# Optimization experiments

Hardware: AMD Instinct MI355X
Metric: run time of the kernel (lower is better)

The kernel has to match this reference:

```python
import jax, jax.numpy as jnp
import numpy as np

NEG_INF = -100000000.0  # matches masked_fill value in torch source

def setup_inputs() -> dict:
    key = jax.random.key(0)
    ks = jax.random.split(key, 7)
    d_model, d = 1024, 128
    B, S = 4, 2048
    scale = 1.0 / np.sqrt(d_model)
    x = jax.random.normal(ks[0], (B, S, d_model), dtype=jnp.float32)
    Wq = jax.random.normal(ks[1], (d, d_model), dtype=jnp.float32) * scale
    bq = jax.random.normal(ks[2], (d,), dtype=jnp.float32) * 0.02
    Wk = jax.random.normal(ks[3], (d, d_model), dtype=jnp.float32) * scale
    bk = jax.random.normal(ks[4], (d,), dtype=jnp.float32) * 0.02
    Wv = jax.random.normal(ks[5], (d, d_model), dtype=jnp.float32) * scale
    bv = jax.random.normal(ks[6], (d,), dtype=jnp.float32) * 0.02
    return {"x": x, "Wq": Wq, "bq": bq, "Wk": Wk, "bk": bk, "Wv": Wv, "bv": bv}

def reference(x, Wq, bq, Wk, bk, Wv, bv):
    # Q,K,V: [B,S,d] via torch Linear (x @ W.T + b)
    Q = jnp.einsum('bsm,dm->bsd', x, Wq) + bq
    K = jnp.einsum('bsm,dm->bsd', x, Wk) + bk
    V = jnp.einsum('bsm,dm->bsd', x, Wv) + bv
    d = Wk.shape[0]
    scale = 1.0 / jnp.sqrt(jnp.asarray(d, dtype=Q.dtype))
    scores = jnp.einsum('bqd,bkd->bqk', Q, K) * scale  # [B,S,S]
    # Faithful to source: tril then value-based mask (tril==0 -> -1e8).
    tril = jnp.tril(scores)
    masked = jnp.where(tril == 0, NEG_INF, tril)
    attn = jax.nn.softmax(masked, axis=-1)
    context = jnp.einsum('bqk,bkd->bqd', attn, V)
    return context
```

## Files before the change

kernel.cpp:

```cpp
#include <hip/hip_runtime.h>

typedef __attribute__((ext_vector_type(8))) short bf16x8;
typedef __attribute__((ext_vector_type(4))) float f32x4;

__device__ __forceinline__ unsigned short f2bf(float f) {
    unsigned int u = __float_as_uint(f);
    u += 0x7fffu + ((u >> 16) & 1u);
    return (unsigned short)(u >> 16);
}
__device__ __forceinline__ float bf2f(unsigned short h) {
    return __uint_as_float((unsigned int)h << 16);
}
__device__ __forceinline__ unsigned int pack2bf(float lo, float hi) {
    return (unsigned int)f2bf(lo) | ((unsigned int)f2bf(hi) << 16);
}
__device__ __forceinline__ unsigned int cvtpk(float a, float b) {
    unsigned int r;
    asm("v_cvt_pk_bf16_f32 %0, %1, %2" : "=v"(r) : "v"(a), "v"(b));
    return r;
}
__device__ __forceinline__ void async_ld16(void* lds, const void* g) {
    __builtin_amdgcn_global_load_lds(
        (const __attribute__((address_space(1))) unsigned int*)g,
        (__attribute__((address_space(3))) unsigned int*)lds, 16, 0, 0);
}

__global__ __launch_bounds__(256) void conv_w(
    const float* __restrict__ Wq, const float* __restrict__ Wk,
    const float* __restrict__ Wv, unsigned short* __restrict__ Wcat)
{
    size_t o = ((size_t)blockIdx.x * 256 + threadIdx.x) * 8;
    int sel = (int)(o >> 17);
    const float* W = (sel == 0) ? Wq : ((sel == 1) ? Wk : Wv);
    const float* src = W + (o & 131071);
    float4 f0 = ((const float4*)src)[0];
    float4 f1 = ((const float4*)src)[1];
    uint4 u;
    u.x = pack2bf(f0.x, f0.y); u.y = pack2bf(f0.z, f0.w);
    u.z = pack2bf(f1.x, f1.y); u.w = pack2bf(f1.z, f1.w);
    *(uint4*)(Wcat + o) = u;
}

__global__ __launch_bounds__(256, 3) void qkv_gemm(
    const float* __restrict__ x,
    const unsigned short* __restrict__ Wcat,
    const float* __restrict__ bq, const float* __restrict__ bk,
    const float* __restrict__ bv,
    unsigned short* __restrict__ Qf,
    unsigned short* __restrict__ Kf,
    unsigned short* __restrict__ Vf)
{
    __shared__ float Asf[2][32 * 64];
    __shared__ unsigned short Bs[2][128 * 64];

    const int tid  = threadIdx.x;
    const int lane = tid & 63;
    const int w    = tid >> 6;
    const int quad = lane >> 4;
    const int ln   = lane & 15;
    const int lr   = lane >> 3;
    const int csw  = ((lane & 7) ^ lr) * 8;

    const int bid   = blockIdx.x;
    const int nb    = bid >> 8;
    const int mbase = (bid & 255) * 32;
    const unsigned short* Wsel = Wcat + (size_t)nb * 128 * 1024;

    const int g0 = tid, g1 = tid + 256;
    const float* asrc0 = x + (size_t)(mbase + (g0 >> 4)) * 1024
                           + (size_t)(((g0 & 15) ^ ((g0 >> 4) & 15)) * 4);
    const float* asrc1 = x + (size_t)(mbase + (g1 >> 4)) * 1024
                           + (size_t)(((g1 & 15) ^ ((g1 >> 4) & 15)) * 4);

    f32x4 acc[2][2];
#pragma unroll
    for (int mt = 0; mt < 2; mt++)
#pragma unroll
        for (int nt = 0; nt < 2; nt++) acc[mt][nt] = (f32x4){0.f, 0.f, 0.f, 0.f};

    auto stageB = [&](int kb, int p) {
        const int kcol = kb * 64 + csw;
#pragma unroll
        for (int j = 0; j < 4; j++) {
            int chunk = w * 4 + j;
            async_ld16(&Bs[p][chunk * 512 + lane * 8],
                       Wsel + (size_t)(chunk * 8 + lr) * 1024 + kcol);
        }
    };
    auto stageA = [&](int kb, int p) {
        async_ld16(&Asf[p][g0 * 4], asrc0 + kb * 64);
        async_ld16(&Asf[p][g1 * 4], asrc1 + kb * 64);
    };
    auto readA = [&](int p, int mt, int ks) -> bf16x8 {
        const int r = mt * 16 + ln;
        const int J = ks * 4 + quad;
        float4 lo = *(const float4*)&Asf[p][r * 64 + (((2 * J)    ) ^ (r & 15)) * 4];
        float4 hi = *(const float4*)&Asf[p][r * 64 + (((2 * J + 1)) ^ (r & 15)) * 4];
        uint4 u = { cvtpk(lo.x, lo.y), cvtpk(lo.z, lo.w),
                    cvtpk(hi.x, hi.y), cvtpk(hi.z, hi.w) };
        return *reinterpret_cast<const bf16x8*>(&u);
    };

    stageB(0, 0);
    stageA(0, 0);
    __syncthreads();

    for (int kb = 0; kb < 16; kb++) {
        const int p = kb & 1;
        if (kb < 15) {
            stageB(kb + 1, p ^ 1);
            stageA(kb + 1, p ^ 1);
        }
#pragma unroll
        for (int ks = 0; ks < 2; ks++) {
            bf16x8 a[2], b[2];
#pragma unroll
            for (int mt = 0; mt < 2; mt++) a[mt] = readA(p, mt, ks);
#pragma unroll
            for (int nt = 0; nt < 2; nt++) {
                int row = w * 32 + nt * 16 + ln;
                b[nt] = *(const bf16x8*)&Bs[p][row * 64 + ((ks * 4 + quad) ^ (ln & 7)) * 8];
            }
#pragma unroll
            for (int mt = 0; mt < 2; mt++)
#pragma unroll
                for (int nt = 0; nt < 2; nt++)
                    acc[mt][nt] = __builtin_amdgcn_mfma_f32_16x16x32_bf16(
                        a[mt], b[nt], acc[mt][nt], 0, 0, 0);
        }
        __syncthreads();
    }

    const float scale = (nb == 0) ? 0.08838834764831845f : 1.0f;
    const float* bsel = (nb == 0) ? bq : ((nb == 1) ? bk : bv);
    float bias_v[2];
#pragma unroll
    for (int nt = 0; nt < 2; nt++) bias_v[nt] = bsel[w * 32 + nt * 16 + ln];

    if (nb == 0) {
#pragma unroll
        for (int mt = 0; mt < 2; mt++)
#pragma unroll
            for (int nt = 0; nt < 2; nt++)
#pragma unroll
                for (int r = 0; r < 4; r++) {
                    int m = mbase + mt * 16 + quad * 4 + r;
                    int d = w * 32 + nt * 16 + ln;
                    int bb = m >> 11, s = m & 2047;
                    int qq = s >> 6, j = s & 63, wv = j >> 4, lnq = j & 15;
                    int ksd = d >> 5, rr = d & 31, qd = rr >> 3, e = rr & 7;
                    size_t idx = (((size_t)((bb * 32 + qq) * 4 + wv) * 4 + ksd) * 64
                                  + qd * 16 + lnq) * 8 + e;
                    Qf[idx] = f2bf((acc[mt][nt][r] + bias_v[nt]) * scale);
                }
    } else if (nb == 1) {
#pragma unroll
        for (int mt = 0; mt < 2; mt++)
#pragma unroll
            for (int nt = 0; nt < 2; nt++)
#pragma unroll
                for (int r = 0; r < 4; r++) {
                    int m = mbase + mt * 16 + quad * 4 + r;
                    int d = w * 32 + nt * 16 + ln;
                    int bb = m >> 11, s = m & 2047;
                    int kt = s >> 6, j = s & 63, ct = j >> 4, lnk = j & 15;
                    int ksd = d >> 5, rr = d & 31, qd = rr >> 3, e = rr & 7;
                    size_t idx = (((size_t)(bb * 128 + kt * 4 + ct) * 4 + ksd) * 64
                                  + qd * 16 + lnk) * 8 + e;
                    Kf[idx] = f2bf(acc[mt][nt][r] + bias_v[nt]);
                }
    } else {
#pragma unroll
        for (int mt = 0; mt < 2; mt++)
#pragma unroll
            for (int nt = 0; nt < 2; nt++) {
                int dd = w * 32 + nt * 16 + ln;
                int m0 = mbase + mt * 16 + quad * 4;
                int bb = m0 >> 11, s0 = m0 & 2047;
                int kt = s0 >> 6, j0 = s0 & 63;
                int kstep = j0 >> 5, rr0 = j0 & 31, qdv = rr0 >> 3, e0 = rr0 & 7;
                int dt = dd >> 4, lnv = dd & 15;
                size_t base = ((((size_t)(bb * 32 + kt) * 2 + kstep) * 8 + dt) * 64
                               + qdv * 16 + lnv) * 8 + e0;
                ushort4 u = { f2bf(acc[mt][nt][0] + bias_v[nt]),
                              f2bf(acc[mt][nt][1] + bias_v[nt]),
                              f2bf(acc[mt][nt][2] + bias_v[nt]),
                              f2bf(acc[mt][nt][3] + bias_v[nt]) };
                *(ushort4*)&Vf[base] = u;
            }
    }
}

__global__ __launch_bounds__(64, 2) void flash_attn(
    const unsigned short* __restrict__ Qf,
    const unsigned short* __restrict__ Kf,
    const unsigned short* __restrict__ Vf,
    unsigned short* __restrict__ Opart,
    float* __restrict__ lsum_g,
    float* __restrict__ out)
{
    __shared__ unsigned short Pl[16][72];

    const int w = blockIdx.x & 3;
    int j = blockIdx.x >> 2;
    const int b = j / 144;
    int t = j % 144;
    int q = 0, c = 0;
#pragma unroll 1
    for (int qq = 0; qq < 32; qq++) {
        int ncq = (qq >> 2) + 1;
        if (t < ncq) { q = qq; c = t; break; }
        t -= ncq;
    }
    const int m4 = q >> 2, r4 = q & 3;
    const int nc = m4 + 1;
    const int pbase = b * 144 + q + 2 * m4 * (m4 - 1) + r4 * m4;
    const int pidx  = pbase + c;
    const int k0 = c * 4;
    const int kend = (c * 4 + 4 < q + 1) ? (c * 4 + 4) : (q + 1);

    const int lane = threadIdx.x & 63, quad = lane >> 4, ln = lane & 15;
    const float M0 = 16.0f;

    bf16x8 qa[4];
    const unsigned short* qbt =
        Qf + (size_t)((b * 32 + q) * 4 + w) * 2048 + lane * 8;
#pragma unroll
    for (int ks = 0; ks < 4; ks++)
        qa[ks] = *(const bf16x8*)(qbt + (size_t)ks * 512);

    float l_i[4];
    f32x4 Ofr[8];
#pragma unroll
    for (int r = 0; r < 4; r++) l_i[r] = 0.f;
#pragma unroll
    for (int dt = 0; dt < 8; dt++) Ofr[dt] = (f32x4){0.f, 0.f, 0.f, 0.f};

    for (int kt = k0; kt < kend; kt++) {
        const unsigned short* kbt = Kf + (size_t)(b * 128 + kt * 4) * 2048 + lane * 8;
        const unsigned short* vbt = Vf + (size_t)(b * 32 + kt) * 8192 + lane * 8;
        bf16x8 kf[4][4], vf[2][8];
#pragma unroll
        for (int ct = 0; ct < 4; ct++)
#pragma unroll
            for (int ks = 0; ks < 4; ks++)
                kf[ct][ks] = *(const bf16x8*)(kbt + (size_t)(ct * 4 + ks) * 512);
#pragma unroll
        for (int kstep = 0; kstep < 2; kstep++)
#pragma unroll
            for (int dt = 0; dt < 8; dt++)
                vf[kstep][dt] = *(const bf16x8*)(vbt + (size_t)(kstep * 8 + dt) * 512);

        f32x4 sfr[4];
#pragma unroll
        for (int ct = 0; ct < 4; ct++) {
            f32x4 s = (f32x4){0.f, 0.f, 0.f, 0.f};
#pragma unroll
            for (int ks = 0; ks < 4; ks++)
                s = __builtin_amdgcn_mfma_f32_16x16x32_bf16(qa[ks], kf[ct][ks], s, 0, 0, 0);
            sfr[ct] = s;
        }

        if (kt == q) {
#pragma unroll
            for (int ct = 0; ct < 4; ct++)
#pragma unroll
                for (int r = 0; r < 4; r++)
                    if (ct * 16 + ln > w * 16 + quad * 4 + r)
                        sfr[ct][r] = -__builtin_inff();
        }

#pragma unroll
        for (int ct = 0; ct < 4; ct++)
#pragma unroll
            for (int r = 0; r < 4; r++) {
                float pv = __expf(sfr[ct][r] - M0);
                l_i[r] += pv;
                Pl[quad * 4 + r][ct * 16 + ln] = f2bf(pv);
            }

#pragma unroll
        for (int kstep = 0; kstep < 2; kstep++) {
            bf16x8 pa = *(const bf16x8*)&Pl[ln][kstep * 32 + quad * 8];
#pragma unroll
            for (int dt = 0; dt < 8; dt++)
                Ofr[dt] = __builtin_amdgcn_mfma_f32_16x16x32_bf16(pa, vf[kstep][dt], Ofr[dt], 0, 0, 0);
        }
    }

#pragma unroll
    for (int off = 1; off < 16; off <<= 1)
#pragma unroll
        for (int r = 0; r < 4; r++) l_i[r] += __shfl_xor(l_i[r], off, 64);

    if (nc == 1) {
        float inv_[4];
#pragma unroll
        for (int r = 0; r < 4; r++) inv_[r] = 1.0f / l_i[r];
#pragma unroll
        for (int dt = 0; dt < 8; dt++)
#pragma unroll
            for (int r = 0; r < 4; r++) {
                int row = w * 16 + quad * 4 + r;
                out[((size_t)(b * 2048 + q * 64 + row)) * 128 + dt * 16 + ln] =
                    Ofr[dt][r] * inv_[r];
            }
        return;
    }

#pragma unroll
    for (int dt = 0; dt < 8; dt++) {
        ushort4 u = { f2bf(Ofr[dt][0]), f2bf(Ofr[dt][1]),
                      f2bf(Ofr[dt][2]), f2bf(Ofr[dt][3]) };
        *(ushort4*)&Opart[(((size_t)pidx * 8 + dt) * 4 + w) * 256 + lane * 4] = u;
    }
    if (ln == 0) {
#pragma unroll
        for (int r = 0; r < 4; r++)
            lsum_g[(size_t)pidx * 64 + w * 16 + quad * 4 + r] = l_i[r];
    }
}

__global__ __launch_bounds__(256) void combine(
    const unsigned short* __restrict__ Opart,
    const float* __restrict__ lsum_g,
    float* __restrict__ out)
{
    const int j = blockIdx.x;
    const int b = j / 28;
    const int q = (j % 28) + 4;
    const int m4 = q >> 2, r4 = q & 3;
    const int nc = m4 + 1;
    const int pbase = b * 144 + q + 2 * m4 * (m4 - 1) + r4 * m4;

    const int tid  = threadIdx.x;
    const int lane = tid & 63, w = tid >> 6, quad = lane >> 4, ln = lane & 15;

    float lt[4] = {0.f, 0.f, 0.f, 0.f};
    f32x4 Ofr[8];
#pragma unroll
    for (int dt = 0; dt < 8; dt++) Ofr[dt] = (f32x4){0.f, 0.f, 0.f, 0.f};

#pragma unroll 1
    for (int c2 = 0; c2 < nc; c2++) {
        const size_t pb2 = (size_t)(pbase + c2);
#pragma unroll
        for (int r = 0; r < 4; r++)
            lt[r] += lsum_g[pb2 * 64 + w * 16 + quad * 4 + r];
#pragma unroll
        for (int dt = 0; dt < 8; dt++) {
            ushort4 u = *(const ushort4*)&Opart[((pb2 * 8 + dt) * 4 + w) * 256 + lane * 4];
            Ofr[dt][0] += bf2f(u.x);
            Ofr[dt][1] += bf2f(u.y);
            Ofr[dt][2] += bf2f(u.z);
            Ofr[dt][3] += bf2f(u.w);
        }
    }
    float inv_[4];
#pragma unroll
    for (int r = 0; r < 4; r++) inv_[r] = 1.0f / lt[r];
#pragma unroll
    for (int dt = 0; dt < 8; dt++)
#pragma unroll
        for (int r = 0; r < 4; r++) {
            int row = w * 16 + quad * 4 + r;
            out[((size_t)(b * 2048 + q * 64 + row)) * 128 + dt * 16 + ln] =
                Ofr[dt][r] * inv_[r];
        }
}

extern "C" void kernel_launch(void* const* d_in, const int* in_sizes, int n_in,
                              void* d_out, int out_size, void* d_ws, size_t ws_size,
                              hipStream_t stream) {
    const float* x  = (const float*)d_in[0];
    const float* Wq = (const float*)d_in[1];
    const float* bq = (const float*)d_in[2];
    const float* Wk = (const float*)d_in[3];
    const float* bk = (const float*)d_in[4];
    const float* Wv = (const float*)d_in[5];
    const float* bv = (const float*)d_in[6];
    float* out = (float*)d_out;

    char* wsb = (char*)d_ws;
    unsigned short* Opart = (unsigned short*)wsb;
    float*          lsum  = (float*)(wsb + 9437184);
    unsigned short* Wcat  = (unsigned short*)(wsb + 10485760);
    unsigned short* Qf    = (unsigned short*)(wsb + 11272192);
    unsigned short* Kf    = Qf + (size_t)8192 * 128;
    unsigned short* Vf    = Qf + (size_t)2 * 8192 * 128;

    conv_w<<<192, 256, 0, stream>>>(Wq, Wk, Wv, Wcat);
    qkv_gemm<<<768, 256, 0, stream>>>(x, Wcat, bq, bk, bv, Qf, Kf, Vf);
    flash_attn<<<2304, 64, 0, stream>>>(Qf, Kf, Vf, Opart, lsum, out);
    combine<<<112, 256, 0, stream>>>(Opart, lsum, out);
}
```

Baseline: 118.8 us.

## Stage x via registers with bf16 conversion before LDS in QKV GEMM

The QKV projection now loads fp32 x tiles into registers, converts them to bf16 once, and writes them to a swizzled bf16 LDS buffer. Previously the fp32 tiles were async-copied to LDS and each wave converted them on every read. This halves A-tile LDS footprint and removes redundant conversions across the four waves, but the global load is now synchronous through registers instead of async direct-to-LDS. The launch-bounds occupancy hint is also dropped, and the weight conversion kernel now uses the packed bf16 convert instruction.

```diff
diff --git a/kernel.cpp b/kernel.cpp
--- a/kernel.cpp
+++ b/kernel.cpp
@@ -10,9 +10,6 @@
 }
 __device__ __forceinline__ float bf2f(unsigned short h) {
     return __uint_as_float((unsigned int)h << 16);
-}
-__device__ __forceinline__ unsigned int pack2bf(float lo, float hi) {
-    return (unsigned int)f2bf(lo) | ((unsigned int)f2bf(hi) << 16);
 }
 __device__ __forceinline__ unsigned int cvtpk(float a, float b) {
     unsigned int r;
@@ -36,12 +33,12 @@
     float4 f0 = ((const float4*)src)[0];
     float4 f1 = ((const float4*)src)[1];
     uint4 u;
-    u.x = pack2bf(f0.x, f0.y); u.y = pack2bf(f0.z, f0.w);
-    u.z = pack2bf(f1.x, f1.y); u.w = pack2bf(f1.z, f1.w);
+    u.x = cvtpk(f0.x, f0.y); u.y = cvtpk(f0.z, f0.w);
+    u.z = cvtpk(f1.x, f1.y); u.w = cvtpk(f1.z, f1.w);
     *(uint4*)(Wcat + o) = u;
 }
 
-__global__ __launch_bounds__(256, 3) void qkv_gemm(
+__global__ __launch_bounds__(256) void qkv_gemm(
     const float* __restrict__ x,
     const unsigned short* __restrict__ Wcat,
     const float* __restrict__ bq, const float* __restrict__ bk,
@@ -50,7 +47,7 @@
     unsigned short* __restrict__ Kf,
     unsigned short* __restrict__ Vf)
 {
-    __shared__ float Asf[2][32 * 64];
+    __shared__ unsigned short As[2][32 * 64];
     __shared__ unsigned short Bs[2][128 * 64];
 
     const int tid  = threadIdx.x;
@@ -66,11 +63,12 @@
     const int mbase = (bid & 255) * 32;
     const unsigned short* Wsel = Wcat + (size_t)nb * 128 * 1024;
 
-    const int g0 = tid, g1 = tid + 256;
-    const float* asrc0 = x + (size_t)(mbase + (g0 >> 4)) * 1024
-                           + (size_t)(((g0 & 15) ^ ((g0 >> 4) & 15)) * 4);
-    const float* asrc1 = x + (size_t)(mbase + (g1 >> 4)) * 1024
-                           + (size_t)(((g1 & 15) ^ ((g1 >> 4) & 15)) * 4);
+    const int arow  = tid >> 3;
+    const int achk  = tid & 7;
+    const int aslot = achk ^ (arow & 7);
+    const float* xsrc = x + (size_t)(mbase + arow) * 1024 + achk * 8;
+    unsigned short* adst0 = &As[0][arow * 64 + aslot * 8];
+    unsigned short* adst1 = &As[1][arow * 64 + aslot * 8];
 
     f32x4 acc[2][2];
 #pragma unroll
@@ -87,35 +85,36 @@
                        Wsel + (size_t)(chunk * 8 + lr) * 1024 + kcol);
         }
     };
-    auto stageA = [&](int kb, int p) {
-        async_ld16(&Asf[p][g0 * 4], asrc0 + kb * 64);
-        async_ld16(&Asf[p][g1 * 4], asrc1 + kb * 64);
+    auto writeA = [&](int p, const float4& f0, const float4& f1) {
+        uint4 u;
+        u.x = cvtpk(f0.x, f0.y); u.y = cvtpk(f0.z, f0.w);
+        u.z = cvtpk(f1.x, f1.y); u.w = cvtpk(f1.z, f1.w);
+        *(uint4*)((p == 0) ? adst0 : adst1) = u;
     };
-    auto readA = [&](int p, int mt, int ks) -> bf16x8 {
-        const int r = mt * 16 + ln;
-        const int J = ks * 4 + quad;
-        float4 lo = *(const float4*)&Asf[p][r * 64 + (((2 * J)    ) ^ (r & 15)) * 4];
-        float4 hi = *(const float4*)&Asf[p][r * 64 + (((2 * J + 1)) ^ (r & 15)) * 4];
-        uint4 u = { cvtpk(lo.x, lo.y), cvtpk(lo.z, lo.w),
-                    cvtpk(hi.x, hi.y), cvtpk(hi.z, hi.w) };
-        return *reinterpret_cast<const bf16x8*>(&u);
-    };
-
+
+    float4 a0 = ((const float4*)xsrc)[0];
+    float4 a1 = ((const float4*)xsrc)[1];
     stageB(0, 0);
-    stageA(0, 0);
+    writeA(0, a0, a1);
     __syncthreads();
 
     for (int kb = 0; kb < 16; kb++) {
         const int p = kb & 1;
+        float4 n0, n1;
         if (kb < 15) {
             stageB(kb + 1, p ^ 1);
-            stageA(kb + 1, p ^ 1);
+            const float* xs = xsrc + (kb + 1) * 64;
+            n0 = ((const float4*)xs)[0];
+            n1 = ((const float4*)xs)[1];
         }
 #pragma unroll
         for (int ks = 0; ks < 2; ks++) {
             bf16x8 a[2], b[2];
 #pragma unroll
-            for (int mt = 0; mt < 2; mt++) a[mt] = readA(p, mt, ks);
+            for (int mt = 0; mt < 2; mt++) {
+                int row = mt * 16 + ln;
+                a[mt] = *(const bf16x8*)&As[p][row * 64 + ((ks * 4 + quad) ^ (ln & 7)) * 8];
+            }
 #pragma unroll
             for (int nt = 0; nt < 2; nt++) {
                 int row = w * 32 + nt * 16 + ln;
@@ -128,6 +127,7 @@
                     acc[mt][nt] = __builtin_amdgcn_mfma_f32_16x16x32_bf16(
                         a[mt], b[nt], acc[mt][nt], 0, 0, 0);
         }
+        if (kb < 15) writeA(p ^ 1, n0, n1);
         __syncthreads();
     }
 
```

Result: no change. 121.0 us (+1.8%).

## Split QKV GEMM tile across 8 waves and use hardware bf16 pack in weight conversion

Applied to the files above, without the earlier changes.

The QKV projection GEMM block grows from 4 to 8 waves arranged 2x4 over the same 32x128 output tile, so each wave computes one 16-row strip with two MFMA accumulators instead of four. Each thread now issues half as many async global-to-LDS loads per stage. The aim is more latency hiding and better spread of staging work, at the cost of more waves per block and lower MFMA work per wave. The weight conversion kernel also switches from software rounding to the v_cvt_pk_bf16_f32 instruction.

```diff
diff --git a/kernel.cpp b/kernel.cpp
--- a/kernel.cpp
+++ b/kernel.cpp
@@ -10,9 +10,6 @@
 }
 __device__ __forceinline__ float bf2f(unsigned short h) {
     return __uint_as_float((unsigned int)h << 16);
-}
-__device__ __forceinline__ unsigned int pack2bf(float lo, float hi) {
-    return (unsigned int)f2bf(lo) | ((unsigned int)f2bf(hi) << 16);
 }
 __device__ __forceinline__ unsigned int cvtpk(float a, float b) {
     unsigned int r;
@@ -36,12 +33,12 @@
     float4 f0 = ((const float4*)src)[0];
     float4 f1 = ((const float4*)src)[1];
     uint4 u;
-    u.x = pack2bf(f0.x, f0.y); u.y = pack2bf(f0.z, f0.w);
-    u.z = pack2bf(f1.x, f1.y); u.w = pack2bf(f1.z, f1.w);
+    u.x = cvtpk(f0.x, f0.y); u.y = cvtpk(f0.z, f0.w);
+    u.z = cvtpk(f1.x, f1.y); u.w = cvtpk(f1.z, f1.w);
     *(uint4*)(Wcat + o) = u;
 }
 
-__global__ __launch_bounds__(256, 3) void qkv_gemm(
+__global__ __launch_bounds__(512, 4) void qkv_gemm(
     const float* __restrict__ x,
     const unsigned short* __restrict__ Wcat,
     const float* __restrict__ bq, const float* __restrict__ bk,
@@ -56,6 +53,8 @@
     const int tid  = threadIdx.x;
     const int lane = tid & 63;
     const int w    = tid >> 6;
+    const int wm   = w >> 2;
+    const int wn   = w & 3;
     const int quad = lane >> 4;
     const int ln   = lane & 15;
     const int lr   = lane >> 3;
@@ -64,35 +63,30 @@
     const int bid   = blockIdx.x;
     const int nb    = bid >> 8;
     const int mbase = (bid & 255) * 32;
-    const unsigned short* Wsel = Wcat + (size_t)nb * 128 * 1024;
-
-    const int g0 = tid, g1 = tid + 256;
-    const float* asrc0 = x + (size_t)(mbase + (g0 >> 4)) * 1024
-                           + (size_t)(((g0 & 15) ^ ((g0 >> 4) & 15)) * 4);
-    const float* asrc1 = x + (size_t)(mbase + (g1 >> 4)) * 1024
-                           + (size_t)(((g1 & 15) ^ ((g1 >> 4) & 15)) * 4);
-
-    f32x4 acc[2][2];
-#pragma unroll
-    for (int mt = 0; mt < 2; mt++)
-#pragma unroll
-        for (int nt = 0; nt < 2; nt++) acc[mt][nt] = (f32x4){0.f, 0.f, 0.f, 0.f};
+    const unsigned short* Wsel = Wcat + (size_t)nb * 131072;
+
+    const int g = tid;
+    const float* asrc = x + (size_t)(mbase + (g >> 4)) * 1024
+                          + (size_t)(((g & 15) ^ ((g >> 4) & 15)) * 4);
+
+    f32x4 acc[2];
+#pragma unroll
+    for (int nt = 0; nt < 2; nt++) acc[nt] = (f32x4){0.f, 0.f, 0.f, 0.f};
 
     auto stageB = [&](int kb, int p) {
         const int kcol = kb * 64 + csw;
 #pragma unroll
-        for (int j = 0; j < 4; j++) {
-            int chunk = w * 4 + j;
+        for (int j = 0; j < 2; j++) {
+            int chunk = w * 2 + j;
             async_ld16(&Bs[p][chunk * 512 + lane * 8],
                        Wsel + (size_t)(chunk * 8 + lr) * 1024 + kcol);
         }
     };
     auto stageA = [&](int kb, int p) {
-        async_ld16(&Asf[p][g0 * 4], asrc0 + kb * 64);
-        async_ld16(&Asf[p][g1 * 4], asrc1 + kb * 64);
+        async_ld16(&Asf[p][g * 4], asrc + kb * 64);
     };
-    auto readA = [&](int p, int mt, int ks) -> bf16x8 {
-        const int r = mt * 16 + ln;
+    auto readA = [&](int p, int ks) -> bf16x8 {
+        const int r = wm * 16 + ln;
         const int J = ks * 4 + quad;
         float4 lo = *(const float4*)&Asf[p][r * 64 + (((2 * J)    ) ^ (r & 15)) * 4];
         float4 hi = *(const float4*)&Asf[p][r * 64 + (((2 * J + 1)) ^ (r & 15)) * 4];
@@ -113,20 +107,15 @@
         }
 #pragma unroll
         for (int ks = 0; ks < 2; ks++) {
-            bf16x8 a[2], b[2];
-#pragma unroll
-            for (int mt = 0; mt < 2; mt++) a[mt] = readA(p, mt, ks);
-#pragma unroll
-            for (int nt = 0; nt < 2; nt++) {
-                int row = w * 32 + nt * 16 + ln;
-                b[nt] = *(const bf16x8*)&Bs[p][row * 64 + ((ks * 4 + quad) ^ (ln & 7)) * 8];
-            }
-#pragma unroll
-            for (int mt = 0; mt < 2; mt++)
-#pragma unroll
-                for (int nt = 0; nt < 2; nt++)
-                    acc[mt][nt] = __builtin_amdgcn_mfma_f32_16x16x32_bf16(
-                        a[mt], b[nt], acc[mt][nt], 0, 0, 0);
+            const int slot = ((ks * 4 + quad) ^ (ln & 7)) * 8;
+            bf16x8 a = readA(p, ks);
+            bf16x8 b[2];
+#pragma unroll
+            for (int nt = 0; nt < 2; nt++)
+                b[nt] = *(const bf16x8*)&Bs[p][(wn * 32 + nt * 16 + ln) * 64 + slot];
+#pragma unroll
+            for (int nt = 0; nt < 2; nt++)
+                acc[nt] = __builtin_amdgcn_mfma_f32_16x16x32_bf16(a, b[nt], acc[nt], 0, 0, 0);
         }
         __syncthreads();
     }
@@ -135,59 +124,53 @@
     const float* bsel = (nb == 0) ? bq : ((nb == 1) ? bk : bv);
     float bias_v[2];
 #pragma unroll
-    for (int nt = 0; nt < 2; nt++) bias_v[nt] = bsel[w * 32 + nt * 16 + ln];
+    for (int nt = 0; nt < 2; nt++) bias_v[nt] = bsel[wn * 32 + nt * 16 + ln];
 
     if (nb == 0) {
 #pragma unroll
-        for (int mt = 0; mt < 2; mt++)
-#pragma unroll
-            for (int nt = 0; nt < 2; nt++)
-#pragma unroll
-                for (int r = 0; r < 4; r++) {
-                    int m = mbase + mt * 16 + quad * 4 + r;
-                    int d = w * 32 + nt * 16 + ln;
-                    int bb = m >> 11, s = m & 2047;
-                    int qq = s >> 6, j = s & 63, wv = j >> 4, lnq = j & 15;
-                    int ksd = d >> 5, rr = d & 31, qd = rr >> 3, e = rr & 7;
-                    size_t idx = (((size_t)((bb * 32 + qq) * 4 + wv) * 4 + ksd) * 64
-                                  + qd * 16 + lnq) * 8 + e;
-                    Qf[idx] = f2bf((acc[mt][nt][r] + bias_v[nt]) * scale);
-                }
+        for (int nt = 0; nt < 2; nt++)
+#pragma unroll
+            for (int r = 0; r < 4; r++) {
+                int m = mbase + wm * 16 + quad * 4 + r;
+                int d = wn * 32 + nt * 16 + ln;
+                int bb = m >> 11, s = m & 2047;
+                int qq = s >> 6, j = s & 63, wv = j >> 4, lnq = j & 15;
+                int ksd = d >> 5, rr = d & 31, qd = rr >> 3, e = rr & 7;
+                size_t idx = (((size_t)((bb * 32 + qq) * 4 + wv) * 4 + ksd) * 64
+                              + qd * 16 + lnq) * 8 + e;
+                Qf[idx] = f2bf((acc[nt][r] + bias_v[nt]) * scale);
+            }
     } else if (nb == 1) {
 #pragma unroll
-        for (int mt = 0; mt < 2; mt++)
-#pragma unroll
-            for (int nt = 0; nt < 2; nt++)
-#pragma unroll
-                for (int r = 0; r < 4; r++) {
-                    int m = mbase + mt * 16 + quad * 4 + r;
-                    int d = w * 32 + nt * 16 + ln;
-                    int bb = m >> 11, s = m & 2047;
-                    int kt = s >> 6, j = s & 63, ct = j >> 4, lnk = j & 15;
-                    int ksd = d >> 5, rr = d & 31, qd = rr >> 3, e = rr & 7;
-                    size_t idx = (((size_t)(bb * 128 + kt * 4 + ct) * 4 + ksd) * 64
-                                  + qd * 16 + lnk) * 8 + e;
-                    Kf[idx] = f2bf(acc[mt][nt][r] + bias_v[nt]);
-                }
+        for (int nt = 0; nt < 2; nt++)
+#pragma unroll
+            for (int r = 0; r < 4; r++) {
+                int m = mbase + wm * 16 + quad * 4 + r;
+                int d = wn * 32 + nt * 16 + ln;
+                int bb = m >> 11, s = m & 2047;
+                int kt = s >> 6, j = s & 63, ct = j >> 4, lnk = j & 15;
+                int ksd = d >> 5, rr = d & 31, qd = rr >> 3, e = rr & 7;
+                size_t idx = (((size_t)(bb * 128 + kt * 4 + ct) * 4 + ksd) * 64
+                              + qd * 16 + lnk) * 8 + e;
+                Kf[idx] = f2bf(acc[nt][r] + bias_v[nt]);
+            }
     } else {
 #pragma unroll
-        for (int mt = 0; mt < 2; mt++)
-#pragma unroll
-            for (int nt = 0; nt < 2; nt++) {
-                int dd = w * 32 + nt * 16 + ln;
-                int m0 = mbase + mt * 16 + quad * 4;
-                int bb = m0 >> 11, s0 = m0 & 2047;
-                int kt = s0 >> 6, j0 = s0 & 63;
-                int kstep = j0 >> 5, rr0 = j0 & 31, qdv = rr0 >> 3, e0 = rr0 & 7;
-                int dt = dd >> 4, lnv = dd & 15;
-                size_t base = ((((size_t)(bb * 32 + kt) * 2 + kstep) * 8 + dt) * 64
-                               + qdv * 16 + lnv) * 8 + e0;
-                ushort4 u = { f2bf(acc[mt][nt][0] + bias_v[nt]),
-                              f2bf(acc[mt][nt][1] + bias_v[nt]),
-                              f2bf(acc[mt][nt][2] + bias_v[nt]),
-                              f2bf(acc[mt][nt][3] + bias_v[nt]) };
-                *(ushort4*)&Vf[base] = u;
-            }
+        for (int nt = 0; nt < 2; nt++) {
+            int dd = wn * 32 + nt * 16 + ln;
+            int m0 = mbase + wm * 16 + quad * 4;
+            int bb = m0 >> 11, s0 = m0 & 2047;
+            int kt = s0 >> 6, j0 = s0 & 63;
+            int kstep = j0 >> 5, rr0 = j0 & 31, qdv = rr0 >> 3, e0 = rr0 & 7;
+            int dt = dd >> 4, lnv = dd & 15;
+            size_t base = ((((size_t)(bb * 32 + kt) * 2 + kstep) * 8 + dt) * 64
+                           + qdv * 16 + lnv) * 8 + e0;
+            ushort4 u = { f2bf(acc[nt][0] + bias_v[nt]),
+                          f2bf(acc[nt][1] + bias_v[nt]),
+                          f2bf(acc[nt][2] + bias_v[nt]),
+                          f2bf(acc[nt][3] + bias_v[nt]) };
+            *(ushort4*)&Vf[base] = u;
+        }
     }
 }
 
@@ -390,7 +373,7 @@
     unsigned short* Vf    = Qf + (size_t)2 * 8192 * 128;
 
     conv_w<<<192, 256, 0, stream>>>(Wq, Wk, Wv, Wcat);
-    qkv_gemm<<<768, 256, 0, stream>>>(x, Wcat, bq, bk, bv, Qf, Kf, Vf);
+    qkv_gemm<<<768, 512, 0, stream>>>(x, Wcat, bq, bk, bv, Qf, Kf, Vf);
     flash_attn<<<2304, 64, 0, stream>>>(Qf, Kf, Vf, Opart, lsum, out);
     combine<<<112, 256, 0, stream>>>(Opart, lsum, out);
 }
```

New measurement: 117.2 us (median of 2 runs). About the same (-1.4%).
